# Kernel tuning notes

Measured on AMD Instinct MI355X. Metric: run time of the kernel, lower is better.

Reference implementation:

```python
import jax, jax.numpy as jnp
import numpy as np

ALPHA = 0.5
TEMPORAL_UNIT = 0
B, T, D = 8, 1024, 320
TIME_MAX = 10_000_000


def setup_inputs() -> dict:
    key = jax.random.key(0)
    k1, k2, k3 = jax.random.split(key, 3)
    z1 = jax.random.normal(k1, (B, T, D), dtype=jnp.float32)
    z2 = jax.random.normal(k2, (B, T, D), dtype=jnp.float32)
    event_time = jnp.sort(
        jax.random.randint(k3, (B, T), 0, TIME_MAX, dtype=jnp.int32), axis=-1
    )
    return {"z1": z1, "z2": z2, "event_time": event_time}


def _neg_logsoftmax_offdiag(sim):
    # tril(sim,-1)[...,:-1] + triu(sim,1)[...,1:]  -> (.., N, N-1), then -log_softmax
    logits = jnp.tril(sim, -1)[..., :-1] + jnp.triu(sim, 1)[..., 1:]
    return -jax.nn.log_softmax(logits, axis=-1)


def _instance_loss(z1, z2):
    b, t = z1.shape[0], z1.shape[1]
    if b == 1:
        return jnp.float32(0.0)
    z = jnp.concatenate([z1, z2], axis=0).transpose(1, 0, 2)  # (T, 2B, D)
    sim = jnp.einsum('tid,tjd->tij', z, z)                    # (T, 2B, 2B)
    logits = _neg_logsoftmax_offdiag(sim)                     # (T, 2B, 2B-1)
    i = jnp.arange(b)
    return (logits[:, i, b + i - 1].mean() + logits[:, b + i, i].mean()) / 2


def _temporal_loss(z1, z2):
    t = z1.shape[1]
    if t == 1:
        return jnp.float32(0.0)
    z = jnp.concatenate([z1, z2], axis=1)                     # (B, 2T, D)
    sim = jnp.einsum('bid,bjd->bij', z, z)                    # (B, 2T, 2T)
    logits = _neg_logsoftmax_offdiag(sim)                     # (B, 2T, 2T-1)
    ti = jnp.arange(t)
    return (logits[:, ti, t + ti - 1].mean() + logits[:, t + ti, ti].mean()) / 2


def _pool_and_filter(z, time):
    # max_pool1d(kernel=2, stride=1) over time axis
    bsz, seq_len, dim = z.shape
    pooled = jnp.maximum(z[:, :-1], z[:, 1:])                  # (B, T-1, D)
    pooled_time = (time[:, :-1] + time[:, 1:]) // 2            # (B, T-1)
    deltas = jnp.diff(time, axis=-1)                           # (B, T-1)
    indices = jnp.argsort(deltas, axis=-1)                     # permutation of 0..T-2
    mask = indices < seq_len // 2                              # exactly T//2 Trues/row
    tm1 = seq_len - 1
    ar = jnp.arange(tm1)
    # stable in-order selection of masked positions: masked keys keep their index,
    # unmasked keys are pushed past the end; sort + take first T//2
    sel = jnp.sort(jnp.where(mask, ar, ar + tm1), axis=-1)[:, : seq_len // 2]
    pooled = jnp.take_along_axis(pooled, sel[:, :, None], axis=1)
    pooled_time = jnp.take_along_axis(pooled_time, sel, axis=1)
    return pooled, pooled_time


def _hier_loss(z1, z2, time, alpha=ALPHA, temporal_unit=TEMPORAL_UNIT):
    loss = jnp.float32(0.0)
    d = 0
    while z1.shape[1] > 1:  # static Python loop over hierarchy levels
        if alpha != 0:
            loss = loss + alpha * _instance_loss(z1, z2)
        if d >= temporal_unit and (1 - alpha) != 0:
            loss = loss + (1 - alpha) * _temporal_loss(z1, z2)
        d += 1
        z1, _ = _pool_and_filter(z1, time)
        z2, time = _pool_and_filter(z2, time)
    if z1.shape[1] == 1:
        if alpha != 0:
            loss = loss + alpha * _instance_loss(z1, z2)
        d += 1
    return loss / d


def reference(z1, z2, event_time):
    return _hier_loss(z1, z2, event_time)
```

## Files before the change

kernel.cpp:

```cpp
#include <hip/hip_runtime.h>
#include <cstdint>
#include <cstddef>

#define D_DIM 320
#define NEGINF (-1e30f)

typedef __attribute__((ext_vector_type(8))) short bf16x8_t;
typedef __attribute__((ext_vector_type(4))) float f32x4_t;
typedef __attribute__((ext_vector_type(16))) float f32x16_t;

struct Tab {
  int T[11], S[11], zoff[11], wsoff[11];
  int tileStart[12], instStart[12], rstart[12];
  float scale[11];
  int totTemp, totInst, totr;
};

__device__ __forceinline__ float bf2f(unsigned short u) {
  union { unsigned int i; float f; } v; v.i = ((unsigned int)u) << 16; return v.f;
}
__device__ __forceinline__ unsigned short f2bf(float f) {
  union { float f; unsigned int i; } u; u.f = f;
  unsigned int b = u.i + 0x7FFFu + ((u.i >> 16) & 1u);
  return (unsigned short)(b >> 16);
}

__device__ __forceinline__ const unsigned short* zrowb(
    const unsigned short* __restrict__ z1, const unsigned short* __restrict__ z2,
    int b, int T, int r) {
  return (r < T) ? (z1 + ((size_t)b * T + r) * D_DIM)
                 : (z2 + ((size_t)b * T + (r - T)) * D_DIM);
}

#define GLOAD_LDS16(SRC, DST)                                                   \
  __builtin_amdgcn_global_load_lds(                                             \
      (const __attribute__((address_space(1))) void*)(SRC),                     \
      (__attribute__((address_space(3))) void*)(DST), 16, 0, 0)

#define BUF1 8192
#define BUF2 16384

#define STAGE(koff, bufofs)                                                     \
    do {                                                                        \
      GLOAD_LDS16(gA0 + (koff), dA0 + (bufofs));                                \
      GLOAD_LDS16(gA1 + (koff), dA1 + (bufofs));                                \
      GLOAD_LDS16(gB0 + (koff), dB0 + (bufofs));                                \
      GLOAD_LDS16(gB1 + (koff), dB1 + (bufofs));                                \
    } while (0)

#define PHASE3(k, bo, bo2, VM, DO_PF)                                           \
    do {                                                                        \
      asm volatile("s_waitcnt vmcnt(" #VM ")" ::: "memory");                    \
      __builtin_amdgcn_s_barrier();                                             \
      if (DO_PF) STAGE((k + 2) * 32, bo2);                                      \
      bf16x8_t af[4], bfr[4];                                                   \
      _Pragma("unroll")                                                         \
      for (int at = 0; at < 4; ++at)                                            \
        af[at] = *(const bf16x8_t*)(vA + (bo) + at * 128);                      \
      _Pragma("unroll")                                                         \
      for (int ct = 0; ct < 4; ++ct)                                            \
        bfr[ct] = *(const bf16x8_t*)(vB + (bo) + ct * 128);                     \
      asm volatile("s_waitcnt lgkmcnt(0)" ::: "memory");                        \
      __builtin_amdgcn_sched_barrier(0);                                        \
      __builtin_amdgcn_s_setprio(1);                                            \
      _Pragma("unroll")                                                         \
      for (int ct = 0; ct < 4; ++ct)                                            \
        _Pragma("unroll")                                                       \
        for (int at = 0; at < 4; ++at)                                          \
          acc[at][ct] = __builtin_amdgcn_mfma_f32_16x16x32_bf16(                \
              af[at], bfr[ct], acc[at][ct], 0, 0, 0);                           \
      __builtin_amdgcn_s_setprio(0);                                            \
    } while (0)

__device__ __forceinline__ void tile_body(
    unsigned char* smem, int tid,
    const unsigned short* zz1, const unsigned short* zz2,
    int b, int T, int S, int rb, int sg,
    float* wm, float* wv) {
  int N = 2 * T;
  int row0 = rb * 128, col0 = sg * 128;
  int w = tid >> 6, lane = tid & 63;
  int lq = lane >> 4, lr = lane & 15;
  int wr = w >> 1, wc = w & 1;

  unsigned short* lds = (unsigned short*)smem;

  int ra0 = row0 + lane;        if (ra0 > N - 1) ra0 = N - 1;
  int ra1 = row0 + 64 + lane;   if (ra1 > N - 1) ra1 = N - 1;
  int ca0 = col0 + lane;        if (ca0 > N - 1) ca0 = N - 1;
  int ca1 = col0 + 64 + lane;   if (ca1 > N - 1) ca1 = N - 1;
  const unsigned short* gA0 = zrowb(zz1, zz2, b, T, ra0) + w * 8;
  const unsigned short* gA1 = zrowb(zz1, zz2, b, T, ra1) + w * 8;
  const unsigned short* gB0 = zrowb(zz1, zz2, b, T, ca0) + w * 8;
  const unsigned short* gB1 = zrowb(zz1, zz2, b, T, ca1) + w * 8;
  unsigned short* dA0 = &lds[((w) * 128 + lane) * 8];
  unsigned short* dA1 = &lds[((w) * 128 + 64 + lane) * 8];
  unsigned short* dB0 = &lds[((4 + w) * 128 + lane) * 8];
  unsigned short* dB1 = &lds[((4 + w) * 128 + 64 + lane) * 8];

  f32x4_t acc[4][4];
#pragma unroll
  for (int at = 0; at < 4; ++at)
#pragma unroll
    for (int ct = 0; ct < 4; ++ct) acc[at][ct] = (f32x4_t)(0.f);

  const unsigned short* vA = &lds[((lq) * 128 + wr * 64 + lr) * 8];
  const unsigned short* vB = &lds[((4 + lq) * 128 + wc * 64 + lr) * 8];

  STAGE(0, 0);
  STAGE(32, BUF1);
  PHASE3(0, 0,    BUF2, 4, 1);
  PHASE3(1, BUF1, 0,    4, 1);
  PHASE3(2, BUF2, BUF1, 4, 1);
  PHASE3(3, 0,    BUF2, 4, 1);
  PHASE3(4, BUF1, 0,    4, 1);
  PHASE3(5, BUF2, BUF1, 4, 1);
  PHASE3(6, 0,    BUF2, 4, 1);
  PHASE3(7, BUF1, 0,    4, 1);
  PHASE3(8, BUF2, 0,    4, 0);
  PHASE3(9, 0,    0,    0, 0);
  __builtin_amdgcn_s_barrier();

  float (*mS)[128] = (float(*)[128])(smem);
  float (*sS)[128] = (float(*)[128])(smem + 1024);
  float (*mC)[128] = (float(*)[128])(smem + 2048);
  float (*sC)[128] = (float(*)[128])(smem + 3072);

#pragma unroll
  for (int at = 0; at < 4; ++at) {
#pragma unroll
    for (int rg = 0; rg < 4; ++rg) {
      int rloc = wr * 64 + at * 16 + lq * 4 + rg;
      int rglob = row0 + rloc;
      float v[4];
#pragma unroll
      for (int ct = 0; ct < 4; ++ct) {
        int cg = col0 + wc * 64 + ct * 16 + lr;
        v[ct] = (cg < N && cg != rglob) ? acc[at][ct][rg] : NEGINF;
      }
      float m = fmaxf(fmaxf(v[0], v[1]), fmaxf(v[2], v[3]));
#pragma unroll
      for (int o = 1; o < 16; o <<= 1) m = fmaxf(m, __shfl_xor(m, o));
      float sv = __expf(v[0] - m) + __expf(v[1] - m) +
                 __expf(v[2] - m) + __expf(v[3] - m);
#pragma unroll
      for (int o = 1; o < 16; o <<= 1) sv += __shfl_xor(sv, o);
      if (lr == 0) { mS[wc][rloc] = m; sS[wc][rloc] = sv; }
    }
  }
  if (rb != sg) {
#pragma unroll
    for (int ct = 0; ct < 4; ++ct) {
      float m = NEGINF;
#pragma unroll
      for (int at = 0; at < 4; ++at)
#pragma unroll
        for (int rg = 0; rg < 4; ++rg) m = fmaxf(m, acc[at][ct][rg]);
      m = fmaxf(m, __shfl_xor(m, 16));
      m = fmaxf(m, __shfl_xor(m, 32));
      float s = 0.f;
#pragma unroll
      for (int at = 0; at < 4; ++at)
#pragma unroll
        for (int rg = 0; rg < 4; ++rg) s += __expf(acc[at][ct][rg] - m);
      s += __shfl_xor(s, 16);
      s += __shfl_xor(s, 32);
      if (lq == 0) {
        mC[wr][wc * 64 + ct * 16 + lr] = m;
        sC[wr][wc * 64 + ct * 16 + lr] = s;
      }
    }
  }
  __syncthreads();

  if (tid < 128) {
    int rglob = row0 + tid;
    if (rglob < N) {
      float m0 = mS[0][tid], m1 = mS[1][tid];
      float m = fmaxf(m0, m1);
      float sv = sS[0][tid] * __expf(m0 - m) + sS[1][tid] * __expf(m1 - m);
      int idx = (b * S + sg) * N + rglob;
      wm[idx] = m;
      wv[idx] = sv;
    }
    if (rb != sg) {
      float m0 = mC[0][tid], m1 = mC[1][tid];
      float m = fmaxf(m0, m1);
      float sv = sC[0][tid] * __expf(m0 - m) + sC[1][tid] * __expf(m1 - m);
      int idx = (b * S + rb) * N + col0 + tid;
      wm[idx] = m;
      wv[idx] = sv;
    }
  }
}

__device__ __forceinline__ float inst_wave(
    const unsigned short* zz1, const unsigned short* zz2, int T, int t, int lane) {
  int lq = lane >> 4, lr = lane & 15;
  const unsigned short* zr = (lr < 8)
      ? zz1 + ((size_t)lr * T + t) * D_DIM
      : zz2 + ((size_t)(lr - 8) * T + t) * D_DIM;
  zr += lq * 8;
  f32x4_t c = (f32x4_t)(0.f);
#pragma unroll
  for (int k = 0; k < 10; ++k) {
    bf16x8_t a = *(const bf16x8_t*)(zr + k * 32);
    c = __builtin_amdgcn_mfma_f32_16x16x32_bf16(a, a, c, 0, 0, 0);
  }
  float lsum = 0.f;
#pragma unroll
  for (int rg = 0; rg < 4; ++rg) {
    int rrow = lq * 4 + rg;
    float v = c[rg];
    float x = (lr != rrow) ? v : NEGINF;
    float m = x;
#pragma unroll
    for (int o = 1; o < 16; o <<= 1) m = fmaxf(m, __shfl_xor(m, o));
    float s = __expf(x - m);
#pragma unroll
    for (int o = 1; o < 16; o <<= 1) s += __shfl_xor(s, o);
    int pos = (rrow < 8) ? rrow + 8 : rrow - 8;
    if (lr == pos) lsum += m + __logf(s) - v;
  }
#pragma unroll
  for (int o = 1; o < 64; o <<= 1) lsum += __shfl_xor(lsum, o);
  return lsum;
}

__global__ __launch_bounds__(256) void convert_kernel(
    const float* __restrict__ i1, const float* __restrict__ i2,
    unsigned short* __restrict__ o1, unsigned short* __restrict__ o2,
    int n4, float* __restrict__ out, int outn) {
  int i = blockIdx.x * 256 + threadIdx.x;
  if (i < outn) out[i] = 0.f;
  int stride = gridDim.x * 256;
  for (int j = i; j < n4; j += stride) {
    float4 v = ((const float4*)i1)[j];
    ushort4 r;
    r.x = f2bf(v.x); r.y = f2bf(v.y); r.z = f2bf(v.z); r.w = f2bf(v.w);
    ((ushort4*)o1)[j] = r;
    float4 u = ((const float4*)i2)[j];
    ushort4 q;
    q.x = f2bf(u.x); q.y = f2bf(u.y); q.z = f2bf(u.z); q.w = f2bf(u.w);
    ((ushort4*)o2)[j] = q;
  }
}

__global__ __launch_bounds__(256, 3) void work0_kernel(
    const int* __restrict__ time0,
    const unsigned short* __restrict__ z1, const unsigned short* __restrict__ z2,
    float* __restrict__ wsm, float* __restrict__ wss,
    float* __restrict__ wsInst,
    int* __restrict__ SET0, int* __restrict__ L0LEN,
    int* __restrict__ SET5, int* __restrict__ L5LEN) {
  __shared__ __align__(16) unsigned char smem[49152];
  int bx = blockIdx.x;
  int tid = threadIdx.x;

  if (bx < 8) {
    int b = bx;
    int lane = tid & 63, wid = tid >> 6;
    int* tcur = (int*)smem;
    unsigned* hist = (unsigned*)(smem + 4096);
    unsigned* cum = (unsigned*)(smem + 8192);
    unsigned long long* arr = (unsigned long long*)(smem + 12288);
    int* sortedIdx = (int*)(smem + 20480);
    int* tnew = (int*)(smem + 24576);
    int* srcK = (int*)(smem + 26624);
    int* setA = (int*)(smem + 28672);
    int* setB = (int*)(smem + 32768);
    int* lenA = (int*)(smem + 36864);
    int* lenB = (int*)(smem + 40960);
    unsigned* minW = (unsigned*)(smem + 43008);
    unsigned* maxW = (unsigned*)(smem + 43072);
    unsigned* wsum = (unsigned*)(smem + 43136);
    int* wcnt = (int*)(smem + 43200);

#pragma unroll
    for (int i = 0; i < 4; ++i) {
      int e = tid + 256 * i;
      tcur[e] = time0[b * 1024 + e];
      setA[e] = e;
      lenA[e] = 1;
    }
    __syncthreads();

    int pp = 0;
    for (int lvl = 1; lvl <= 10; ++lvl) {
      int T = 2048 >> lvl;
      int n = T - 1, half = T >> 1;
      bool act[4];
      int dd[4];
      unsigned bkey[4];
      unsigned mn = 0xFFFFFFFFu, mx = 0u;
#pragma unroll
      for (int i = 0; i < 4; ++i) {
        int e = tid + 256 * i;
        act[i] = e < n;
        dd[i] = 0; bkey[i] = 0;
        if (act[i]) {
          dd[i] = tcur[e + 1] - tcur[e];
          bkey[i] = __float_as_uint((float)dd[i]);
          mn = mn < bkey[i] ? mn : bkey[i];
          mx = mx > bkey[i] ? mx : bkey[i];
        }
        hist[e] = 0;
      }
#pragma unroll
      for (int o = 1; o < 64; o <<= 1) {
        unsigned m2 = (unsigned)__shfl_xor((int)mn, o);
        unsigned x2 = (unsigned)__shfl_xor((int)mx, o);
        mn = mn < m2 ? mn : m2;
        mx = mx > x2 ? mx : x2;
      }
      if (lane == 0) { minW[wid] = mn; maxW[wid] = mx; }
      __syncthreads();

      unsigned bmin = 0xFFFFFFFFu, bmax = 0;
#pragma unroll
      for (int i = 0; i < 4; ++i) {
        bmin = bmin < minW[i] ? bmin : minW[i];
        bmax = bmax > maxW[i] ? bmax : maxW[i];
      }
      unsigned long long range = (unsigned long long)(bmax - bmin) + 1;
      unsigned long long scl = (1024ULL << 30) / range;
      int bkt[4]; unsigned av[4];
#pragma unroll
      for (int i = 0; i < 4; ++i) {
        if (act[i]) {
          int bk = (int)(((unsigned long long)(bkey[i] - bmin) * scl) >> 30);
          bkt[i] = bk > 1023 ? 1023 : bk;
          av[i] = atomicAdd(&hist[bkt[i]], 1u);
        }
      }
      __syncthreads();

      {
        unsigned l0 = hist[4 * tid], l1 = hist[4 * tid + 1],
                 l2 = hist[4 * tid + 2], l3 = hist[4 * tid + 3];
        unsigned s = l0 + l1 + l2 + l3;
        unsigned inc = s;
#pragma unroll
        for (int o = 1; o < 64; o <<= 1) {
          unsigned t = (unsigned)__shfl_up((int)inc, o);
          if (lane >= o) inc += t;
        }
        if (lane == 63) wsum[wid] = inc;
        __syncthreads();
        unsigned wpre = 0;
        for (int j = 0; j < wid; ++j) wpre += wsum[j];
        unsigned ex = wpre + inc - s;
        cum[4 * tid] = ex;
        cum[4 * tid + 1] = ex + l0;
        cum[4 * tid + 2] = ex + l0 + l1;
        cum[4 * tid + 3] = ex + l0 + l1 + l2;
      }
      __syncthreads();

      unsigned long long key[4];
#pragma unroll
      for (int i = 0; i < 4; ++i) {
        if (act[i]) {
          key[i] = ((unsigned long long)(unsigned)dd[i] << 10) |
                   (unsigned)(tid + 256 * i);
          arr[cum[bkt[i]] + av[i]] = key[i];
        }
      }
      __syncthreads();

#pragma unroll
      for (int i = 0; i < 4; ++i) {
        if (act[i]) {
          int base = (int)cum[bkt[i]];
          int occ = (int)hist[bkt[i]];
          int c = 0;
          for (int j = 0; j < occ; ++j) c += (arr[base + j] < key[i]) ? 1 : 0;
          sortedIdx[base + c] = tid + 256 * i;
        }
      }
      __syncthreads();

      bool msk[4]; int rw[4];
#pragma unroll
      for (int i = 0; i < 4; ++i) {
        int k = tid + 256 * i;
        msk[i] = (k < n) && (sortedIdx[k] < half);
        unsigned long long bal = __ballot(msk[i]);
        rw[i] = __popcll(bal & ((1ull << lane) - 1ull));
        if (lane == 0) wcnt[i * 4 + wid] = (int)__popcll(bal);
      }
      __syncthreads();
#pragma unroll
      for (int i = 0; i < 4; ++i) {
        if (msk[i]) {
          int seg = i * 4 + wid;
          int pre = 0;
          for (int j = 0; j < seg; ++j) pre += wcnt[j];
          int rr = pre + rw[i];
          int k = tid + 256 * i;
          srcK[rr] = k;
          tnew[rr] = (tcur[k] + tcur[k + 1]) >> 1;
        }
      }
      __syncthreads();

      if (lvl == 6) {
        int* sp = pp ? setB : setA;
        int* lp = pp ? lenB : lenA;
        if (tid < 32) { sp[tid] = tid; lp[tid] = 1; }
        __syncthreads();
      }
      {
        int ll = (lvl <= 5) ? lvl : (lvl - 5);
        int* sp = pp ? setB : setA;
        int* lp = pp ? lenB : lenA;
        int* sc = pp ? setA : setB;
        int* lc = pp ? lenA : lenB;
        int *gset, *glen;
        if (lvl <= 5) {
          gset = SET0 + b * 5120 + (lvl - 1) * 1024;
          glen = L0LEN + b * 992 + (1024 - (1024 >> (lvl - 1)));
        } else {
          gset = SET5 + b * 160 + (lvl - 6) * 32;
          glen = L5LEN + b * 32 + (32 - (32 >> (lvl - 6)));
        }
        int tmax = half << ll;
#pragma unroll
        for (int i = 0; i < 4; ++i) {
          int s = tid + 256 * i;
          if (s < tmax) {
            int j = s >> ll, e2 = s & ((1 << ll) - 1);
            int k = srcK[j];
            int la = lp[k], lb2 = lp[k + 1];
            int v = -1;
            int sh = ll - 1;
            if (e2 < la) v = sp[(k << sh) + e2];
            else if (e2 < la + lb2) v = sp[((k + 1) << sh) + (e2 - la)];
            if (e2 == 0) { lc[j] = la + lb2; glen[j] = la + lb2; }
            if (v >= 0) { sc[s] = v; gset[s] = v; }
          }
        }
        __syncthreads();
        pp ^= 1;
      }
#pragma unroll
      for (int i = 0; i < 4; ++i) {
        int j = tid + 256 * i;
        if (j < half) tcur[j] = tnew[j];
      }
      __syncthreads();
    }
  } else if (bx < 8 + 1088) {
    const int T = 1024, S = 16;
    int local = bx - 8;
    int b = local % 8;
    int pr = local / 8;
    int rb = 0, tt = pr;
    while (tt >= S - rb) { tt -= S - rb; ++rb; }
    int sg = rb + tt;
    tile_body(smem, tid, z1, z2, b, T, S, rb, sg, wsm, wss);
  } else {
    int iw = (bx - 1096) * 4 + (tid >> 6);
    float lsum = inst_wave(z1, z2, 1024, iw, tid & 63);
    if ((tid & 63) == 0) wsInst[iw] = lsum * (1.0f / 360448.0f);
  }
}

__global__ __launch_bounds__(256) void mat1_kernel(
    unsigned short* __restrict__ z1, unsigned short* __restrict__ z2,
    const int* __restrict__ SET0, const int* __restrict__ L0LEN) {
  int g = blockIdx.x * 256 + threadIdx.x;
  int c = g % 40;
  int t2 = g / 40;
  int rr = t2 % 992;
  int bzi = t2 / 992;
  int b = bzi & 7;
  unsigned short* z = (bzi >> 3) ? z2 : z1;
  int l, j, off0;
  if (rr < 512)      { l = 1; j = rr;       off0 = 0; }
  else if (rr < 768) { l = 2; j = rr - 512; off0 = 512; }
  else if (rr < 896) { l = 3; j = rr - 768; off0 = 768; }
  else if (rr < 960) { l = 4; j = rr - 896; off0 = 896; }
  else               { l = 5; j = rr - 960; off0 = 960; }
  int len = L0LEN[b * 992 + off0 + j];
  const int* st = SET0 + b * 5120 + (l - 1) * 1024 + (j << l);
  const unsigned short* src = z + (size_t)b * 1024 * D_DIM;
  int cc = c * 8;
  bf16x8_t mx = *(const bf16x8_t*)(src + (size_t)st[0] * D_DIM + cc);
  for (int e = 1; e < len; ++e) {
    bf16x8_t a = *(const bf16x8_t*)(src + (size_t)st[e] * D_DIM + cc);
#pragma unroll
    for (int q = 0; q < 8; ++q)
      mx[q] = (bf2f((unsigned short)mx[q]) >= bf2f((unsigned short)a[q])) ? mx[q] : a[q];
  }
  size_t zo = (size_t)2560 * (2048 - (2048 >> l));
  int Tl = 1024 >> l;
  *(bf16x8_t*)(z + zo + ((size_t)b * Tl + j) * D_DIM + cc) = mx;
}

__global__ __launch_bounds__(256, 3) void work45_kernel(
    unsigned short* __restrict__ z1, unsigned short* __restrict__ z2,
    const int* __restrict__ SET5, const int* __restrict__ L5LEN,
    float* __restrict__ wsm, float* __restrict__ wss,
    float* __restrict__ wsInst, Tab tab) {
  __shared__ __align__(16) unsigned char smem[49152];
  int bx = blockIdx.x;
  int tid = threadIdx.x;

  if (bx < 78) {
    int g = bx * 256 + tid;
    if (g >= 2 * 8 * 31 * 40) return;
    int c = g % 40;
    int t2 = g / 40;
    int rr = t2 % 31;
    int bzi = t2 / 31;
    int b = bzi & 7;
    unsigned short* z = (bzi >> 3) ? z2 : z1;
    int l, j, off5;
    if (rr < 16)      { l = 6;  j = rr;      off5 = 0; }
    else if (rr < 24) { l = 7;  j = rr - 16; off5 = 16; }
    else if (rr < 28) { l = 8;  j = rr - 24; off5 = 24; }
    else if (rr < 30) { l = 9;  j = rr - 28; off5 = 28; }
    else              { l = 10; j = rr - 30; off5 = 30; }
    int len = L5LEN[b * 32 + off5 + j];
    const int* st = SET5 + b * 160 + (l - 6) * 32 + (j << (l - 5));
    const unsigned short* src = z + (size_t)2560 * (2048 - 64) + (size_t)b * 32 * D_DIM;
    int cc = c * 8;
    bf16x8_t mx = *(const bf16x8_t*)(src + (size_t)st[0] * D_DIM + cc);
    for (int e = 1; e < len; ++e) {
      bf16x8_t a = *(const bf16x8_t*)(src + (size_t)st[e] * D_DIM + cc);
#pragma unroll
      for (int q = 0; q < 8; ++q)
        mx[q] = (bf2f((unsigned short)mx[q]) >= bf2f((unsigned short)a[q])) ? mx[q] : a[q];
    }
    size_t zo = (size_t)2560 * (2048 - (2048 >> l));
    int Tl = 1024 >> l;
    *(bf16x8_t*)(z + zo + ((size_t)b * Tl + j) * D_DIM + cc) = mx;
  } else if (bx < 486) {
    int g = tab.tileStart[1] + (bx - 78);
    int l = 1;
    while (g >= tab.tileStart[l + 1]) ++l;
    int T = tab.T[l], S = tab.S[l];
    int local = g - tab.tileStart[l];
    int npl = (S * (S + 1)) >> 1;
    int nid = (local % 8) * npl + local / 8;
    int b = nid / npl;
    int pr = nid % npl;
    int rb = 0, tt = pr;
    while (tt >= S - rb) { tt -= S - rb; ++rb; }
    int sg = rb + tt;
    tile_body(smem, tid, z1 + tab.zoff[l], z2 + tab.zoff[l], b, T, S, rb, sg,
              wsm + tab.wsoff[l], wss + tab.wsoff[l]);
  } else {
    int iw = 1024 + (bx - 486) * 4 + (tid >> 6);
    if (iw < 2016) {
      int l = 1;
      while (iw >= tab.instStart[l + 1]) ++l;
      int t = iw - tab.instStart[l];
      float lsum = inst_wave(z1 + tab.zoff[l], z2 + tab.zoff[l], tab.T[l], t,
                             tid & 63);
      if ((tid & 63) == 0) wsInst[iw] = lsum * tab.scale[l];
    }
  }
}

__global__ __launch_bounds__(256) void final_kernel(
    const unsigned short* __restrict__ z1, const unsigned short* __restrict__ z2,
    const float* __restrict__ wsm, const float* __restrict__ wss,
    const float* __restrict__ wsInst, float* __restrict__ out, Tab tab,
    int nc) {
  int bx = blockIdx.x;
  int tid = threadIdx.x;

  if (bx < nc) {
    int g = bx * 256 + tid;
    float loss = 0.f;
    if (g < tab.totr) {
      int l = 0;
      while (g >= tab.rstart[l + 1]) ++l;
      int row = g - tab.rstart[l];
      int T = tab.T[l], N = 2 * T, S = tab.S[l];
      int b = row / N, r = row % N;
      const float* wm = wsm + tab.wsoff[l];
      const float* wv = wss + tab.wsoff[l];
      float m = NEGINF;
      for (int s = 0; s < S; ++s) m = fmaxf(m, wm[(b * S + s) * N + r]);
      float sv = 0.f;
      for (int s = 0; s < S; ++s) {
        int idx = (b * S + s) * N + r;
        sv += wv[idx] * __expf(wm[idx] - m);
      }
      const unsigned short* zz1 = z1 + tab.zoff[l];
      const unsigned short* zz2 = z2 + tab.zoff[l];
      int pos = (r < T) ? r + T : r - T;
      const bf16x8_t* za = (const bf16x8_t*)zrowb(zz1, zz2, b, T, r);
      const bf16x8_t* zp = (const bf16x8_t*)zrowb(zz1, zz2, b, T, pos);
      float dot = 0.f;
      for (int k = 0; k < D_DIM / 8; ++k) {
        bf16x8_t a = za[k], p = zp[k];
#pragma unroll
        for (int e = 0; e < 8; ++e)
          dot += bf2f((unsigned short)a[e]) * bf2f((unsigned short)p[e]);
      }
      loss = (m + logf(sv) - dot) * tab.scale[l];
    } else if (g < tab.totr + 2016) {
      loss = wsInst[g - tab.totr];
    }
    float v = loss;
#pragma unroll
    for (int o = 1; o < 64; o <<= 1) v += __shfl_xor(v, o);
    __shared__ float part[4];
    int w = tid >> 6;
    if ((tid & 63) == 0) part[w] = v;
    __syncthreads();
    if (tid == 0)
      atomicAdd(out, part[0] + part[1] + part[2] + part[3]);
  } else if (bx < nc + 8) {
    int widx = (bx - nc) * 4 + (tid >> 6);
    int l = 6 + (widx >> 3), b = widx & 7;
    int T = tab.T[l], N = 2 * T;
    const unsigned short* zz1 = z1 + tab.zoff[l];
    const unsigned short* zz2 = z2 + tab.zoff[l];
    int lane = tid & 63;
    int col = lane & 31, h = lane >> 5;
    int rl = (col < N) ? col : 0;
    const unsigned short* rowp = (rl < T)
        ? zz1 + ((size_t)b * T + rl) * D_DIM
        : zz2 + ((size_t)b * T + (rl - T)) * D_DIM;
    rowp += h * 8;
    f32x16_t acc = (f32x16_t)(0.f);
#pragma unroll
    for (int m2 = 0; m2 < 20; ++m2) {
      bf16x8_t a = *(const bf16x8_t*)(rowp + m2 * 16);
      acc = __builtin_amdgcn_mfma_f32_32x32x16_bf16(a, a, acc, 0, 0, 0);
    }
    float lsum = 0.f;
#pragma unroll
    for (int rg = 0; rg < 16; ++rg) {
      int row = (rg & 3) + 8 * (rg >> 2) + 4 * h;
      float x = acc[rg];
      float xm = (col < N && row < N && col != row) ? x : NEGINF;
      float m = xm;
#pragma unroll
      for (int o = 1; o < 32; o <<= 1) m = fmaxf(m, __shfl_xor(m, o));
      float s = __expf(xm - m);
#pragma unroll
      for (int o = 1; o < 32; o <<= 1) s += __shfl_xor(s, o);
      int pos = (row < T) ? row + T : row - T;
      if (row < N && col == pos) lsum += m + __logf(s) - x;
    }
#pragma unroll
    for (int o = 1; o < 64; o <<= 1) lsum += __shfl_xor(lsum, o);
    if (lane == 0) atomicAdd(out, lsum * tab.scale[l]);
  } else {
    int widx = (bx - nc - 8) * 4 + (tid >> 6);
    if (widx < 31) {
      int iw = 2016 + widx;
      int l = 6;
      while (iw >= tab.instStart[l + 1]) ++l;
      int t = iw - tab.instStart[l];
      float lsum = inst_wave(z1 + tab.zoff[l], z2 + tab.zoff[l], tab.T[l], t,
                             tid & 63);
      if ((tid & 63) == 0) atomicAdd(out, lsum * tab.scale[l]);
    }
  }
}

extern "C" void kernel_launch(void* const* d_in, const int* in_sizes, int n_in,
                              void* d_out, int out_size, void* d_ws, size_t ws_size,
                              hipStream_t stream) {
  const float* z1_in = (const float*)d_in[0];
  const float* z2_in = (const float*)d_in[1];
  const int* time_in = (const int*)d_in[2];
  float* out = (float*)d_out;

  Tab tab;
  int zo = 0, wso = 0, ts = 0, is = 0, rs = 0;
  for (int l = 0; l < 11; ++l) {
    int T = 1024 >> l, N = 2 * T;
    int S = (N >= 128) ? N / 128 : 1;
    tab.T[l] = T;
    tab.S[l] = S;
    tab.zoff[l] = zo;
    tab.scale[l] = 1.0f / (352.0f * (float)T);
    tab.tileStart[l] = ts;
    tab.instStart[l] = is;
    tab.wsoff[l] = (T > 1) ? wso : 0;
    tab.rstart[l] = rs;
    if (T > 1) {
      ts += 8 * ((S * (S + 1)) >> 1);
      wso += 8 * S * N;
      if (l <= 5) rs += 8 * N;
    }
    is += T;
    zo += 8 * T * D_DIM;
  }
  tab.tileStart[11] = ts;
  tab.instStart[11] = is;
  tab.rstart[11] = rs;
  for (int l = 6; l <= 11; ++l) tab.rstart[l] = rs;
  tab.totTemp = ts;
  tab.totInst = is;
  tab.totr = rs;

  char* w = (char*)d_ws;
  unsigned short* z1s = (unsigned short*)w; w += (size_t)zo * 2;
  unsigned short* z2s = (unsigned short*)w; w += (size_t)zo * 2;
  float* wsm = (float*)w; w += (size_t)wso * sizeof(float);
  float* wss = (float*)w; w += (size_t)wso * sizeof(float);
  float* wsInst = (float*)w; w += (size_t)is * sizeof(float);
  int* SET0 = (int*)w; w += (size_t)8 * 5120 * sizeof(int);
  int* L0LEN = (int*)w; w += (size_t)8 * 992 * sizeof(int);
  int* SET5 = (int*)w; w += (size_t)8 * 160 * sizeof(int);
  int* L5LEN = (int*)w; w += (size_t)8 * 32 * sizeof(int);

  int n0 = 8 * 1024 * D_DIM;
  convert_kernel<<<2048, 256, 0, stream>>>(z1_in, z2_in, z1s, z2s, n0 / 4,
                                           out, out_size);
  work0_kernel<<<8 + 1088 + 256, 256, 0, stream>>>(
      time_in, z1s, z2s, wsm, wss, wsInst, SET0, L0LEN, SET5, L5LEN);
  mat1_kernel<<<2480, 256, 0, stream>>>(z1s, z2s, SET0, L0LEN);
  work45_kernel<<<78 + 408 + 248, 256, 0, stream>>>(
      z1s, z2s, SET5, L5LEN, wsm, wss, wsInst, tab);
  int nc = (tab.totr + 2016 + 255) / 256;
  final_kernel<<<nc + 16, 256, 0, stream>>>(z1s, z2s, wsm, wss, wsInst, out,
                                            tab, nc);
}
```

Baseline: 113.7 us.

## Regroup kernel stages to merge conversion with selection and pooling with level-0 tiles

Reorganises the launch schedule from five kernels to four. The fp32-to-bf16 conversion now runs in the same launch as the per-batch time-selection blocks. The level-1..5 max-pool gather now runs in the same launch as the level-0 temporal tiles and instance waves, and the level 6-10 pooling is moved after the level 1-5 tiles. This removes one kernel boundary and lets independent work share the GPU. The pooling blocks in the second kernel read level-0 bf16 data written by the first kernel, so correctness relies on the launch ordering between kernels, as before.

```diff
diff --git a/kernel.cpp b/kernel.cpp
--- a/kernel.cpp
+++ b/kernel.cpp
@@ -227,33 +227,14 @@
   return lsum;
 }
 
-__global__ __launch_bounds__(256) void convert_kernel(
+__global__ __launch_bounds__(256) void l1_kernel(
+    const int* __restrict__ time0,
     const float* __restrict__ i1, const float* __restrict__ i2,
     unsigned short* __restrict__ o1, unsigned short* __restrict__ o2,
-    int n4, float* __restrict__ out, int outn) {
-  int i = blockIdx.x * 256 + threadIdx.x;
-  if (i < outn) out[i] = 0.f;
-  int stride = gridDim.x * 256;
-  for (int j = i; j < n4; j += stride) {
-    float4 v = ((const float4*)i1)[j];
-    ushort4 r;
-    r.x = f2bf(v.x); r.y = f2bf(v.y); r.z = f2bf(v.z); r.w = f2bf(v.w);
-    ((ushort4*)o1)[j] = r;
-    float4 u = ((const float4*)i2)[j];
-    ushort4 q;
-    q.x = f2bf(u.x); q.y = f2bf(u.y); q.z = f2bf(u.z); q.w = f2bf(u.w);
-    ((ushort4*)o2)[j] = q;
-  }
-}
-
-__global__ __launch_bounds__(256, 3) void work0_kernel(
-    const int* __restrict__ time0,
-    const unsigned short* __restrict__ z1, const unsigned short* __restrict__ z2,
-    float* __restrict__ wsm, float* __restrict__ wss,
-    float* __restrict__ wsInst,
+    int n4, float* __restrict__ out, int outn, int nconv,
     int* __restrict__ SET0, int* __restrict__ L0LEN,
     int* __restrict__ SET5, int* __restrict__ L5LEN) {
-  __shared__ __align__(16) unsigned char smem[49152];
+  __shared__ __align__(16) unsigned char smem[43264];
   int bx = blockIdx.x;
   int tid = threadIdx.x;
 
@@ -450,55 +431,76 @@
       }
       __syncthreads();
     }
-  } else if (bx < 8 + 1088) {
+  } else {
+    int i = (bx - 8) * 256 + tid;
+    if (i < outn) out[i] = 0.f;
+    int stride = nconv * 256;
+    for (int j = i; j < n4; j += stride) {
+      float4 v = ((const float4*)i1)[j];
+      ushort4 r;
+      r.x = f2bf(v.x); r.y = f2bf(v.y); r.z = f2bf(v.z); r.w = f2bf(v.w);
+      ((ushort4*)o1)[j] = r;
+      float4 u = ((const float4*)i2)[j];
+      ushort4 q;
+      q.x = f2bf(u.x); q.y = f2bf(u.y); q.z = f2bf(u.z); q.w = f2bf(u.w);
+      ((ushort4*)o2)[j] = q;
+    }
+  }
+}
+
+__global__ __launch_bounds__(256, 3) void l2_kernel(
+    unsigned short* __restrict__ z1, unsigned short* __restrict__ z2,
+    float* __restrict__ wsm, float* __restrict__ wss,
+    float* __restrict__ wsInst,
+    const int* __restrict__ SET0, const int* __restrict__ L0LEN) {
+  __shared__ __align__(16) unsigned char smem[49152];
+  int bx = blockIdx.x;
+  int tid = threadIdx.x;
+
+  if (bx < 1088) {
     const int T = 1024, S = 16;
-    int local = bx - 8;
-    int b = local % 8;
-    int pr = local / 8;
+    int b = bx % 8;
+    int pr = bx / 8;
     int rb = 0, tt = pr;
     while (tt >= S - rb) { tt -= S - rb; ++rb; }
     int sg = rb + tt;
     tile_body(smem, tid, z1, z2, b, T, S, rb, sg, wsm, wss);
-  } else {
-    int iw = (bx - 1096) * 4 + (tid >> 6);
+  } else if (bx < 1344) {
+    int iw = (bx - 1088) * 4 + (tid >> 6);
     float lsum = inst_wave(z1, z2, 1024, iw, tid & 63);
     if ((tid & 63) == 0) wsInst[iw] = lsum * (1.0f / 360448.0f);
-  }
-}
-
-__global__ __launch_bounds__(256) void mat1_kernel(
-    unsigned short* __restrict__ z1, unsigned short* __restrict__ z2,
-    const int* __restrict__ SET0, const int* __restrict__ L0LEN) {
-  int g = blockIdx.x * 256 + threadIdx.x;
-  int c = g % 40;
-  int t2 = g / 40;
-  int rr = t2 % 992;
-  int bzi = t2 / 992;
-  int b = bzi & 7;
-  unsigned short* z = (bzi >> 3) ? z2 : z1;
-  int l, j, off0;
-  if (rr < 512)      { l = 1; j = rr;       off0 = 0; }
-  else if (rr < 768) { l = 2; j = rr - 512; off0 = 512; }
-  else if (rr < 896) { l = 3; j = rr - 768; off0 = 768; }
-  else if (rr < 960) { l = 4; j = rr - 896; off0 = 896; }
-  else               { l = 5; j = rr - 960; off0 = 960; }
-  int len = L0LEN[b * 992 + off0 + j];
-  const int* st = SET0 + b * 5120 + (l - 1) * 1024 + (j << l);
-  const unsigned short* src = z + (size_t)b * 1024 * D_DIM;
-  int cc = c * 8;
-  bf16x8_t mx = *(const bf16x8_t*)(src + (size_t)st[0] * D_DIM + cc);
-  for (int e = 1; e < len; ++e) {
-    bf16x8_t a = *(const bf16x8_t*)(src + (size_t)st[e] * D_DIM + cc);
-#pragma unroll
-    for (int q = 0; q < 8; ++q)
-      mx[q] = (bf2f((unsigned short)mx[q]) >= bf2f((unsigned short)a[q])) ? mx[q] : a[q];
-  }
-  size_t zo = (size_t)2560 * (2048 - (2048 >> l));
-  int Tl = 1024 >> l;
-  *(bf16x8_t*)(z + zo + ((size_t)b * Tl + j) * D_DIM + cc) = mx;
-}
-
-__global__ __launch_bounds__(256, 3) void work45_kernel(
+  } else {
+    int g = (bx - 1344) * 256 + tid;
+    int c = g % 40;
+    int t2 = g / 40;
+    int rr = t2 % 992;
+    int bzi = t2 / 992;
+    int b = bzi & 7;
+    unsigned short* z = (bzi >> 3) ? z2 : z1;
+    int l, j, off0;
+    if (rr < 512)      { l = 1; j = rr;       off0 = 0; }
+    else if (rr < 768) { l = 2; j = rr - 512; off0 = 512; }
+    else if (rr < 896) { l = 3; j = rr - 768; off0 = 768; }
+    else if (rr < 960) { l = 4; j = rr - 896; off0 = 896; }
+    else               { l = 5; j = rr - 960; off0 = 960; }
+    int len = L0LEN[b * 992 + off0 + j];
+    const int* st = SET0 + b * 5120 + (l - 1) * 1024 + (j << l);
+    const unsigned short* src = z + (size_t)b * 1024 * D_DIM;
+    int cc = c * 8;
+    bf16x8_t mx = *(const bf16x8_t*)(src + (size_t)st[0] * D_DIM + cc);
+    for (int e = 1; e < len; ++e) {
+      bf16x8_t a = *(const bf16x8_t*)(src + (size_t)st[e] * D_DIM + cc);
+#pragma unroll
+      for (int q = 0; q < 8; ++q)
+        mx[q] = (bf2f((unsigned short)mx[q]) >= bf2f((unsigned short)a[q])) ? mx[q] : a[q];
+    }
+    size_t zo = (size_t)2560 * (2048 - (2048 >> l));
+    int Tl = 1024 >> l;
+    *(bf16x8_t*)(z + zo + ((size_t)b * Tl + j) * D_DIM + cc) = mx;
+  }
+}
+
+__global__ __launch_bounds__(256, 3) void l3_kernel(
     unsigned short* __restrict__ z1, unsigned short* __restrict__ z2,
     const int* __restrict__ SET5, const int* __restrict__ L5LEN,
     float* __restrict__ wsm, float* __restrict__ wss,
@@ -507,8 +509,23 @@
   int bx = blockIdx.x;
   int tid = threadIdx.x;
 
-  if (bx < 78) {
-    int g = bx * 256 + tid;
+  if (bx < 408) {
+    int g = tab.tileStart[1] + bx;
+    int l = 1;
+    while (g >= tab.tileStart[l + 1]) ++l;
+    int T = tab.T[l], S = tab.S[l];
+    int local = g - tab.tileStart[l];
+    int npl = (S * (S + 1)) >> 1;
+    int nid = (local % 8) * npl + local / 8;
+    int b = nid / npl;
+    int pr = nid % npl;
+    int rb = 0, tt = pr;
+    while (tt >= S - rb) { tt -= S - rb; ++rb; }
+    int sg = rb + tt;
+    tile_body(smem, tid, z1 + tab.zoff[l], z2 + tab.zoff[l], b, T, S, rb, sg,
+              wsm + tab.wsoff[l], wss + tab.wsoff[l]);
+  } else if (bx < 486) {
+    int g = (bx - 408) * 256 + tid;
     if (g >= 2 * 8 * 31 * 40) return;
     int c = g % 40;
     int t2 = g / 40;
@@ -536,21 +553,6 @@
     size_t zo = (size_t)2560 * (2048 - (2048 >> l));
     int Tl = 1024 >> l;
     *(bf16x8_t*)(z + zo + ((size_t)b * Tl + j) * D_DIM + cc) = mx;
-  } else if (bx < 486) {
-    int g = tab.tileStart[1] + (bx - 78);
-    int l = 1;
-    while (g >= tab.tileStart[l + 1]) ++l;
-    int T = tab.T[l], S = tab.S[l];
-    int local = g - tab.tileStart[l];
-    int npl = (S * (S + 1)) >> 1;
-    int nid = (local % 8) * npl + local / 8;
-    int b = nid / npl;
-    int pr = nid % npl;
-    int rb = 0, tt = pr;
-    while (tt >= S - rb) { tt -= S - rb; ++rb; }
-    int sg = rb + tt;
-    tile_body(smem, tid, z1 + tab.zoff[l], z2 + tab.zoff[l], b, T, S, rb, sg,
-              wsm + tab.wsoff[l], wss + tab.wsoff[l]);
   } else {
     int iw = 1024 + (bx - 486) * 4 + (tid >> 6);
     if (iw < 2016) {
@@ -697,7 +699,6 @@
   }
   tab.tileStart[11] = ts;
   tab.instStart[11] = is;
-  tab.rstart[11] = rs;
   for (int l = 6; l <= 11; ++l) tab.rstart[l] = rs;
   tab.totTemp = ts;
   tab.totInst = is;
@@ -715,13 +716,14 @@
   int* L5LEN = (int*)w; w += (size_t)8 * 32 * sizeof(int);
 
   int n0 = 8 * 1024 * D_DIM;
-  convert_kernel<<<2048, 256, 0, stream>>>(z1_in, z2_in, z1s, z2s, n0 / 4,
-                                           out, out_size);
-  work0_kernel<<<8 + 1088 + 256, 256, 0, stream>>>(
-      time_in, z1s, z2s, wsm, wss, wsInst, SET0, L0LEN, SET5, L5LEN);
-  mat1_kernel<<<2480, 256, 0, stream>>>(z1s, z2s, SET0, L0LEN);
-  work45_kernel<<<78 + 408 + 248, 256, 0, stream>>>(
-      z1s, z2s, SET5, L5LEN, wsm, wss, wsInst, tab);
+  int nconv = 2040;
+  l1_kernel<<<8 + nconv, 256, 0, stream>>>(time_in, z1_in, z2_in, z1s, z2s,
+                                           n0 / 4, out, out_size, nconv,
+                                           SET0, L0LEN, SET5, L5LEN);
+  l2_kernel<<<1088 + 256 + 2480, 256, 0, stream>>>(z1s, z2s, wsm, wss, wsInst,
+                                                   SET0, L0LEN);
+  l3_kernel<<<408 + 78 + 248, 256, 0, stream>>>(z1s, z2s, SET5, L5LEN,
+                                                wsm, wss, wsInst, tab);
   int nc = (tab.totr + 2016 + 255) / 256;
   final_kernel<<<nc + 16, 256, 0, stream>>>(z1s, z2s, wsm, wss, wsInst, out,
                                             tab, nc);
```

Result: slower. 133.6 us (+17.5%).

## Move level-0 row combine into work45 kernel and reorder its block roles

Applied to the files above, without the earlier changes.

The level-0 temporal row reduction (16384 rows: max/sum over partial softmax stats plus positive-pair dot) moves out of the final kernel into 64 extra blocks of the renamed work45 kernel. Those blocks add into the output with atomics, which shrinks the final kernel's serial tail. Tile blocks are reordered to launch first. The rank-counting loop in the sort is restructured to interleave the four per-thread keys in one loop. The added atomics and reordering could change scheduling balance, and the relocated rows read workspace whose producer ordering must still hold.

```diff
diff --git a/kernel.cpp b/kernel.cpp
--- a/kernel.cpp
+++ b/kernel.cpp
@@ -227,6 +227,44 @@
   return lsum;
 }
 
+__device__ __forceinline__ void combine_rows(
+    const unsigned short* zz1, const unsigned short* zz2,
+    const float* wm, const float* wv,
+    int T, int S, float scale, int b, int r, bool valid,
+    float* out, int tid) {
+  int N = 2 * T;
+  float loss = 0.f;
+  if (valid) {
+    float m = NEGINF;
+    for (int s = 0; s < S; ++s) m = fmaxf(m, wm[(b * S + s) * N + r]);
+    float sv = 0.f;
+    for (int s = 0; s < S; ++s) {
+      int idx = (b * S + s) * N + r;
+      sv += wv[idx] * __expf(wm[idx] - m);
+    }
+    int pos = (r < T) ? r + T : r - T;
+    const bf16x8_t* za = (const bf16x8_t*)zrowb(zz1, zz2, b, T, r);
+    const bf16x8_t* zp = (const bf16x8_t*)zrowb(zz1, zz2, b, T, pos);
+    float dot = 0.f;
+    for (int k = 0; k < D_DIM / 8; ++k) {
+      bf16x8_t a = za[k], p = zp[k];
+#pragma unroll
+      for (int e = 0; e < 8; ++e)
+        dot += bf2f((unsigned short)a[e]) * bf2f((unsigned short)p[e]);
+    }
+    loss = (m + logf(sv) - dot) * scale;
+  }
+  float v = loss;
+#pragma unroll
+  for (int o = 1; o < 64; o <<= 1) v += __shfl_xor(v, o);
+  __shared__ float part[4];
+  int w = tid >> 6;
+  if ((tid & 63) == 0) part[w] = v;
+  __syncthreads();
+  if (tid == 0)
+    atomicAdd(out, part[0] + part[1] + part[2] + part[3]);
+}
+
 __global__ __launch_bounds__(256) void convert_kernel(
     const float* __restrict__ i1, const float* __restrict__ i2,
     unsigned short* __restrict__ o1, unsigned short* __restrict__ o2,
@@ -358,26 +396,36 @@
       __syncthreads();
 
       unsigned long long key[4];
+      int base[4], occ[4];
 #pragma unroll
       for (int i = 0; i < 4; ++i) {
+        base[i] = 0; occ[i] = 0;
         if (act[i]) {
           key[i] = ((unsigned long long)(unsigned)dd[i] << 10) |
                    (unsigned)(tid + 256 * i);
-          arr[cum[bkt[i]] + av[i]] = key[i];
+          base[i] = (int)cum[bkt[i]];
+          arr[base[i] + av[i]] = key[i];
         }
       }
       __syncthreads();
 
+      int cnt[4] = {0, 0, 0, 0};
+      int mocc = 0;
 #pragma unroll
       for (int i = 0; i < 4; ++i) {
         if (act[i]) {
-          int base = (int)cum[bkt[i]];
-          int occ = (int)hist[bkt[i]];
-          int c = 0;
-          for (int j = 0; j < occ; ++j) c += (arr[base + j] < key[i]) ? 1 : 0;
-          sortedIdx[base + c] = tid + 256 * i;
+          occ[i] = (int)hist[bkt[i]];
+          mocc = occ[i] > mocc ? occ[i] : mocc;
         }
       }
+      for (int j = 0; j < mocc; ++j) {
+#pragma unroll
+        for (int i = 0; i < 4; ++i)
+          if (j < occ[i]) cnt[i] += (arr[base[i] + j] < key[i]) ? 1 : 0;
+      }
+#pragma unroll
+      for (int i = 0; i < 4; ++i)
+        if (act[i]) sortedIdx[base[i] + cnt[i]] = tid + 256 * i;
       __syncthreads();
 
       bool msk[4]; int rw[4];
@@ -498,17 +546,32 @@
   *(bf16x8_t*)(z + zo + ((size_t)b * Tl + j) * D_DIM + cc) = mx;
 }
 
-__global__ __launch_bounds__(256, 3) void work45_kernel(
+__global__ __launch_bounds__(256, 3) void l3_kernel(
     unsigned short* __restrict__ z1, unsigned short* __restrict__ z2,
     const int* __restrict__ SET5, const int* __restrict__ L5LEN,
     float* __restrict__ wsm, float* __restrict__ wss,
-    float* __restrict__ wsInst, Tab tab) {
+    float* __restrict__ wsInst, float* __restrict__ out, Tab tab) {
   __shared__ __align__(16) unsigned char smem[49152];
   int bx = blockIdx.x;
   int tid = threadIdx.x;
 
-  if (bx < 78) {
-    int g = bx * 256 + tid;
+  if (bx < 408) {
+    int g = tab.tileStart[1] + bx;
+    int l = 1;
+    while (g >= tab.tileStart[l + 1]) ++l;
+    int T = tab.T[l], S = tab.S[l];
+    int local = g - tab.tileStart[l];
+    int npl = (S * (S + 1)) >> 1;
+    int nid = (local % 8) * npl + local / 8;
+    int b = nid / npl;
+    int pr = nid % npl;
+    int rb = 0, tt = pr;
+    while (tt >= S - rb) { tt -= S - rb; ++rb; }
+    int sg = rb + tt;
+    tile_body(smem, tid, z1 + tab.zoff[l], z2 + tab.zoff[l], b, T, S, rb, sg,
+              wsm + tab.wsoff[l], wss + tab.wsoff[l]);
+  } else if (bx < 486) {
+    int g = (bx - 408) * 256 + tid;
     if (g >= 2 * 8 * 31 * 40) return;
     int c = g % 40;
     int t2 = g / 40;
@@ -536,22 +599,7 @@
     size_t zo = (size_t)2560 * (2048 - (2048 >> l));
     int Tl = 1024 >> l;
     *(bf16x8_t*)(z + zo + ((size_t)b * Tl + j) * D_DIM + cc) = mx;
-  } else if (bx < 486) {
-    int g = tab.tileStart[1] + (bx - 78);
-    int l = 1;
-    while (g >= tab.tileStart[l + 1]) ++l;
-    int T = tab.T[l], S = tab.S[l];
-    int local = g - tab.tileStart[l];
-    int npl = (S * (S + 1)) >> 1;
-    int nid = (local % 8) * npl + local / 8;
-    int b = nid / npl;
-    int pr = nid % npl;
-    int rb = 0, tt = pr;
-    while (tt >= S - rb) { tt -= S - rb; ++rb; }
-    int sg = rb + tt;
-    tile_body(smem, tid, z1 + tab.zoff[l], z2 + tab.zoff[l], b, T, S, rb, sg,
-              wsm + tab.wsoff[l], wss + tab.wsoff[l]);
-  } else {
+  } else if (bx < 734) {
     int iw = 1024 + (bx - 486) * 4 + (tid >> 6);
     if (iw < 2016) {
       int l = 1;
@@ -561,6 +609,10 @@
                              tid & 63);
       if ((tid & 63) == 0) wsInst[iw] = lsum * tab.scale[l];
     }
+  } else {
+    int g = (bx - 734) * 256 + tid;
+    int b = g >> 11, r = g & 2047;
+    combine_rows(z1, z2, wsm, wss, 1024, 16, tab.scale[0], b, r, true, out, tid);
   }
 }
 
@@ -573,7 +625,7 @@
   int tid = threadIdx.x;
 
   if (bx < nc) {
-    int g = bx * 256 + tid;
+    int g = bx * 256 + tid + 16384;
     float loss = 0.f;
     if (g < tab.totr) {
       int l = 0;
@@ -697,7 +749,6 @@
   }
   tab.tileStart[11] = ts;
   tab.instStart[11] = is;
-  tab.rstart[11] = rs;
   for (int l = 6; l <= 11; ++l) tab.rstart[l] = rs;
   tab.totTemp = ts;
   tab.totInst = is;
@@ -720,9 +771,9 @@
   work0_kernel<<<8 + 1088 + 256, 256, 0, stream>>>(
       time_in, z1s, z2s, wsm, wss, wsInst, SET0, L0LEN, SET5, L5LEN);
   mat1_kernel<<<2480, 256, 0, stream>>>(z1s, z2s, SET0, L0LEN);
-  work45_kernel<<<78 + 408 + 248, 256, 0, stream>>>(
-      z1s, z2s, SET5, L5LEN, wsm, wss, wsInst, tab);
-  int nc = (tab.totr + 2016 + 255) / 256;
+  l3_kernel<<<408 + 78 + 248 + 64, 256, 0, stream>>>(
+      z1s, z2s, SET5, L5LEN, wsm, wss, wsInst, out, tab);
+  int nc = (tab.totr - 16384 + 2016 + 255) / 256;
   final_kernel<<<nc + 16, 256, 0, stream>>>(z1s, z2s, wsm, wss, wsInst, out,
                                             tab, nc);
 }
```

Result: slower. 123.4 us (+8.6%).
